# Optimization experiments

Hardware: AMD Instinct MI355X
Metric: run time of the kernel (lower is better)

## Reference

```python
import jax, jax.numpy as jnp
import numpy as np

N, C_IN, C_OUT, H, W = 16, 256, 256, 32, 32
K = 9  # 3x3 kernel


def setup_inputs() -> dict:
    key = jax.random.key(0)
    k1, k2, k3 = jax.random.split(key, 3)
    x = jax.random.normal(k1, (N, C_IN, H, W), dtype=jnp.float32)
    # offsets as produced upstream from anchors: (N, H*W, 18)
    offset = jax.random.normal(k2, (N, H * W, 2 * K), dtype=jnp.float32)
    # DeformConv weight (no bias), kaiming-ish scale
    weight = jax.random.normal(k3, (C_OUT, C_IN, 3, 3), dtype=jnp.float32) * 0.02
    return {"x": x, "offset": offset, "weight": weight}


def _deform_conv3x3(x, offset_nchw, weight):
    """DeformConv v1, kernel 3x3, stride 1, padding 1, dilation 1,
    groups=1, deformable_groups=1, zero padding outside borders."""
    n, c, h, w = x.shape
    o = weight.shape[0]
    # offset channel layout: (dy_k, dx_k) pairs for k = 0..8
    off = offset_nchw.reshape(n, K, 2, h, w)
    dy = off[:, :, 0]  # (N,K,H,W)
    dx = off[:, :, 1]
    ky = (jnp.arange(K) // 3 - 1).astype(x.dtype)  # kernel row offsets -1,0,1
    kx = (jnp.arange(K) % 3 - 1).astype(x.dtype)
    base_y = jnp.arange(h, dtype=x.dtype)[None, None, :, None]
    base_x = jnp.arange(w, dtype=x.dtype)[None, None, None, :]
    py = base_y + ky[None, :, None, None] + dy  # (N,K,H,W) sample rows
    px = base_x + kx[None, :, None, None] + dx  # (N,K,H,W) sample cols

    y0 = jnp.floor(py)
    x0 = jnp.floor(px)
    ly = py - y0  # fractional parts
    lx = px - x0

    x_flat = x.reshape(n, c, h * w)

    def corner(yi, xi, wgt):
        valid = (yi >= 0) & (yi <= h - 1) & (xi >= 0) & (xi <= w - 1)
        yc = jnp.clip(yi, 0, h - 1).astype(jnp.int32)
        xc = jnp.clip(xi, 0, w - 1).astype(jnp.int32)
        idx = (yc * w + xc).reshape(n, K * h * w)
        g = jax.vmap(lambda xf, i: xf[:, i])(x_flat, idx)  # (N,C,K*H*W)
        wv = (wgt * valid.astype(x.dtype)).reshape(n, 1, K * h * w)
        return g * wv

    val = (corner(y0, x0, (1 - ly) * (1 - lx))
           + corner(y0, x0 + 1, (1 - ly) * lx)
           + corner(y0 + 1, x0, ly * (1 - lx))
           + corner(y0 + 1, x0 + 1, ly * lx))
    val = val.reshape(n, c, K, h, w)  # sampled im2col columns
    return jnp.einsum('nckhw,ock->nohw', val, weight.reshape(o, c, K))


def reference(x, offset, weight):
    n, _, h, w = x.shape
    assert h * w == offset.shape[1]
    # AdaptiveConv.forward: (N, HW, 18) -> (N, 18, H, W)
    offset_nchw = jnp.transpose(offset, (0, 2, 1)).reshape(n, 2 * K, h, w)
    return _deform_conv3x3(x, offset_nchw, weight)
```

## Files before the change

kernel.cpp:

```cpp
#include <hip/hip_runtime.h>

#define NB   16
#define CIN  256
#define COUT 256
#define HH   32
#define WW   32
#define HW   1024
#define KK   9
#define CK   2304

typedef __bf16 bf16x8 __attribute__((ext_vector_type(8)));
typedef float  f32x4  __attribute__((ext_vector_type(4)));

__device__ __forceinline__ unsigned short f2bf(float f) {
    unsigned int u = __float_as_uint(f);
    u += 0x7FFFu + ((u >> 16) & 1u);
    return (unsigned short)(u >> 16);
}
__device__ __forceinline__ float bfhi(unsigned int u) {
    return __uint_as_float(u & 0xFFFF0000u);
}
__device__ __forceinline__ float bflo(unsigned int u) {
    return __uint_as_float(u << 16);
}

typedef const __attribute__((address_space(1))) void* gas_ptr;
typedef __attribute__((address_space(3))) void* las_ptr;

__device__ __forceinline__ void async16(const void* g, void* l) {
    __builtin_amdgcn_global_load_lds((gas_ptr)g, (las_ptr)l, 16, 0, 0);
}

__global__ __launch_bounds__(256) void wconv_kernel(const float* __restrict__ w,
                                                    unsigned short* __restrict__ wbf) {
    __shared__ float ls[CK];
    const int o = blockIdx.x;
    const float* wo = w + (size_t)o * CK;
#pragma unroll
    for (int i = threadIdx.x; i < CK; i += 256) ls[i] = wo[i];
    __syncthreads();
    unsigned short* dst = wbf + (size_t)o * CK;
#pragma unroll
    for (int i = threadIdx.x; i < CK; i += 256) {
        int k = i >> 8, c = i & 255;
        dst[i] = f2bf(ls[c * KK + k]);
    }
}

__global__ __launch_bounds__(256) void xt_kernel(const float* __restrict__ x,
                                                 unsigned short* __restrict__ xtb) {
    __shared__ float ls[64][65];
    const int c0  = blockIdx.x * 64;
    const int hw0 = blockIdx.y * 64;
    const int n   = blockIdx.z;
    const int t   = threadIdx.x;
    {
        int c = t >> 2, q = t & 3;
        const float4* base = (const float4*)(x + ((size_t)(n * CIN + c0 + c)) * HW + hw0 + q * 16);
#pragma unroll
        for (int j = 0; j < 4; ++j) {
            float4 v = base[j];
            ls[c][q * 16 + j * 4 + 0] = v.x;
            ls[c][q * 16 + j * 4 + 1] = v.y;
            ls[c][q * 16 + j * 4 + 2] = v.z;
            ls[c][q * 16 + j * 4 + 3] = v.w;
        }
    }
    __syncthreads();
    {
        int hw = t >> 2, seg = (t & 3) * 16;
        unsigned int dw[8];
#pragma unroll
        for (int j = 0; j < 8; ++j) {
            float f0 = ls[seg + 2 * j][hw];
            float f1 = ls[seg + 2 * j + 1][hw];
            dw[j] = (unsigned)f2bf(f0) | ((unsigned)f2bf(f1) << 16);
        }
        uint4* dst = (uint4*)(xtb + ((size_t)(n * HW + hw0 + hw)) * CIN + c0 + seg);
        dst[0] = *(uint4*)&dw[0];
        dst[1] = *(uint4*)&dw[4];
    }
}

__global__ __launch_bounds__(512, 2) void fused_kernel(const unsigned short* __restrict__ wbf,
                                                       const unsigned short* __restrict__ xtb,
                                                       const float* __restrict__ off,
                                                       float* __restrict__ out) {
    __shared__ unsigned short As[2][256 * 64];
    __shared__ unsigned short Bs[2][64 * 64];

    const int tid  = threadIdx.x;
    const int wv   = tid >> 6;
    const int lane = tid & 63;
    const int quad = lane >> 4;
    const int l15  = lane & 15;

    const int hw_local = tid >> 3;
    const int seg      = tid & 7;

    const int id  = blockIdx.x;
    const int n   = ((id & 7) << 1) | ((id >> 3) & 1);
    const int hw0 = (id >> 4) * 64;

    const int hw = hw0 + hw_local;
    const int h  = hw >> 5, w = hw & 31;

    const int srow   = lane >> 3;
    const int schunk = (lane & 7) ^ (srow & 7);

    const uint4*  xb4  = (const uint4*)(xtb + (size_t)n * HW * CIN);
    const float2* offp = (const float2*)(off + ((size_t)n * HW + hw) * (2 * KK));

    f32x4 acc[2][4] = {};

    auto setup = [&](int tap, float wg[4], int ix[4]) {
        float2 o = offp[tap];
        float py = (float)(h + tap / 3 - 1) + o.x;
        float px = (float)(w + tap % 3 - 1) + o.y;
        float y0f = floorf(py), x0f = floorf(px);
        float ly = py - y0f, lx = px - x0f;
        int y0 = (int)y0f, x0 = (int)x0f;
#pragma unroll
        for (int c2 = 0; c2 < 4; ++c2) {
            int yy = y0 + (c2 >> 1);
            int xx = x0 + (c2 & 1);
            float wy = (c2 >> 1) ? ly : 1.0f - ly;
            float wx = (c2 & 1) ? lx : 1.0f - lx;
            bool v = (yy >= 0) && (yy < HH) && (xx >= 0) && (xx < WW);
            wg[c2] = v ? wy * wx : 0.0f;
            int yc = yy < 0 ? 0 : (yy > HH - 1 ? HH - 1 : yy);
            int xc = xx < 0 ? 0 : (xx > WW - 1 ? WW - 1 : xx);
            ix[c2] = yc * WW + xc;
        }
    };

    auto loadc = [&](uint4 cr[4], const int ix[4], int s) {
#pragma unroll
        for (int c2 = 0; c2 < 4; ++c2)
            cr[c2] = xb4[(size_t)ix[c2] * 32 + s * 8 + seg];
    };

    auto build = [&](int nb, int ckb, const uint4 cr[4], const float wg[4]) {
#pragma unroll
        for (int j = 0; j < 4; ++j) {
            int rb = wv * 32 + j * 8;
            async16(wbf + (size_t)(rb + srow) * CK + ckb + schunk * 8, &As[nb][rb * 64]);
        }
        unsigned u0[4], u1[4], u2[4], u3[4];
        *(uint4*)u0 = cr[0]; *(uint4*)u1 = cr[1];
        *(uint4*)u2 = cr[2]; *(uint4*)u3 = cr[3];
        unsigned dw[4];
#pragma unroll
        for (int d = 0; d < 4; ++d) {
            float lo = wg[0] * bflo(u0[d]) + wg[1] * bflo(u1[d])
                     + wg[2] * bflo(u2[d]) + wg[3] * bflo(u3[d]);
            float hi = wg[0] * bfhi(u0[d]) + wg[1] * bfhi(u1[d])
                     + wg[2] * bfhi(u2[d]) + wg[3] * bfhi(u3[d]);
            dw[d] = (unsigned)f2bf(lo) | ((unsigned)f2bf(hi) << 16);
        }
        *(uint4*)&Bs[nb][hw_local * 64 + (seg ^ (hw_local & 7)) * 8] = *(uint4*)dw;
    };

    auto mfma_step = [&](int pb) {
        bf16x8 af[2][2], bfr[4][2];
#pragma unroll
        for (int mi = 0; mi < 2; ++mi)
#pragma unroll
            for (int hh = 0; hh < 2; ++hh) {
                int row = wv * 32 + mi * 16 + l15;
                int ch  = (hh * 4 + quad) ^ (row & 7);
                af[mi][hh] = *(const bf16x8*)&As[pb][row * 64 + ch * 8];
            }
#pragma unroll
        for (int ni = 0; ni < 4; ++ni)
#pragma unroll
            for (int hh = 0; hh < 2; ++hh) {
                int row = ni * 16 + l15;
                int ch  = (hh * 4 + quad) ^ (row & 7);
                bfr[ni][hh] = *(const bf16x8*)&Bs[pb][row * 64 + ch * 8];
            }
#pragma unroll
        for (int mi = 0; mi < 2; ++mi)
#pragma unroll
            for (int ni = 0; ni < 4; ++ni) {
                acc[mi][ni] = __builtin_amdgcn_mfma_f32_16x16x32_bf16(af[mi][0], bfr[ni][0], acc[mi][ni], 0, 0, 0);
                acc[mi][ni] = __builtin_amdgcn_mfma_f32_16x16x32_bf16(af[mi][1], bfr[ni][1], acc[mi][ni], 0, 0, 0);
            }
    };

    float wgc[4], wgn[4];
    int   ixc[4], ixn[4];
    uint4 crA[4], crB[4];

    setup(0, wgc, ixc);
    loadc(crA, ixc, 0);
    build(0, 0, crA, wgc);
    loadc(crB, ixc, 1);
    __syncthreads();

    for (int tap = 0; tap < 9; ++tap) {
        const int ckb = tap * 256;
        build(1, ckb + 64, crB, wgc);
        loadc(crA, ixc, 2);
        mfma_step(0);
        __syncthreads();
        build(0, ckb + 128, crA, wgc);
        loadc(crB, ixc, 3);
        mfma_step(1);
        __syncthreads();
        build(1, ckb + 192, crB, wgc);
        if (tap < 8) { setup(tap + 1, wgn, ixn); loadc(crA, ixn, 0); }
        mfma_step(0);
        __syncthreads();
        if (tap < 8) {
            build(0, ckb + 256, crA, wgn);
            loadc(crB, ixn, 1);
#pragma unroll
            for (int c2 = 0; c2 < 4; ++c2) { wgc[c2] = wgn[c2]; ixc[c2] = ixn[c2]; }
            mfma_step(1);
            __syncthreads();
        } else {
            mfma_step(1);
        }
    }

    float* opnt = out + (size_t)n * COUT * HW + hw0;
#pragma unroll
    for (int mi = 0; mi < 2; ++mi)
#pragma unroll
        for (int ni = 0; ni < 4; ++ni) {
            int col = ni * 16 + l15;
#pragma unroll
            for (int rr = 0; rr < 4; ++rr) {
                int row = wv * 32 + mi * 16 + quad * 4 + rr;
                opnt[(size_t)row * HW + col] = acc[mi][ni][rr];
            }
        }
}

extern "C" void kernel_launch(void* const* d_in, const int* in_sizes, int n_in,
                              void* d_out, int out_size, void* d_ws, size_t ws_size,
                              hipStream_t stream) {
    const float* x   = (const float*)d_in[0];
    const float* off = (const float*)d_in[1];
    const float* wt  = (const float*)d_in[2];
    float* out = (float*)d_out;

    unsigned short* wbf = (unsigned short*)d_ws;
    unsigned short* xtb = (unsigned short*)((char*)d_ws + 1179648);

    wconv_kernel<<<256, 256, 0, stream>>>(wt, wbf);
    xt_kernel<<<dim3(4, 16, 16), 256, 0, stream>>>(x, xtb);
    fused_kernel<<<256, 512, 0, stream>>>(wbf, xtb, off, out);
}
```

Measured before the change: 122.3 us.

## Split fused deform-conv kernel into producer and consumer wavefronts

The 8 wavefronts of each block are split into roles. Four producer waves do the offset setup, bilinear gather, B-tile build and async A-tile loads, and four consumer waves run only MFMAs, each covering 64 output rows instead of 32. The goal is to overlap gather and build latency with matrix math through warp specialization. In exchange, each consumer wave doubles its accumulator and fragment registers, only half the waves issue MFMAs, and producers hold eight uint4 prefetch registers per stage.

```diff
diff --git a/kernel.cpp b/kernel.cpp
--- a/kernel.cpp
+++ b/kernel.cpp
@@ -92,28 +92,34 @@
     const int tid  = threadIdx.x;
     const int wv   = tid >> 6;
     const int lane = tid & 63;
-    const int quad = lane >> 4;
-    const int l15  = lane & 15;
-
-    const int hw_local = tid >> 3;
-    const int seg      = tid & 7;
 
     const int id  = blockIdx.x;
     const int n   = ((id & 7) << 1) | ((id >> 3) & 1);
     const int hw0 = (id >> 4) * 64;
 
-    const int hw = hw0 + hw_local;
-    const int h  = hw >> 5, w = hw & 31;
-
+    const bool producer = (wv >= 4);
+
+    const int quad = lane >> 4;
+    const int l15  = lane & 15;
+    f32x4 acc[4][4] = {};
+
+    const int ptid = (wv - 4) * 64 + lane;
+    const int hwl  = ptid >> 2;
+    const int segq = ptid & 3;
+    const int hw   = hw0 + (hwl & 63);
+    const int h    = hw >> 5, w = hw & 31;
+    const int pv   = wv - 4;
     const int srow   = lane >> 3;
     const int schunk = (lane & 7) ^ (srow & 7);
 
     const uint4*  xb4  = (const uint4*)(xtb + (size_t)n * HW * CIN);
     const float2* offp = (const float2*)(off + ((size_t)n * HW + hw) * (2 * KK));
 
-    f32x4 acc[2][4] = {};
-
-    auto setup = [&](int tap, float wg[4], int ix[4]) {
+    float wgs0[4], wgs1[4];
+    uint4 crs0[8], crs1[8];
+
+    auto prefetch = [&](int t, float* wg, uint4* cr) {
+        int tap = t >> 2, sub = t & 3;
         float2 o = offp[tap];
         float py = (float)(h + tap / 3 - 1) + o.x;
         float px = (float)(w + tap % 3 - 1) + o.y;
@@ -130,44 +136,45 @@
             wg[c2] = v ? wy * wx : 0.0f;
             int yc = yy < 0 ? 0 : (yy > HH - 1 ? HH - 1 : yy);
             int xc = xx < 0 ? 0 : (xx > WW - 1 ? WW - 1 : xx);
-            ix[c2] = yc * WW + xc;
+            int ridx = yc * WW + xc;
+            const uint4* rp = xb4 + (size_t)ridx * 32 + sub * 8 + segq * 2;
+            cr[2 * c2]     = rp[0];
+            cr[2 * c2 + 1] = rp[1];
         }
     };
 
-    auto loadc = [&](uint4 cr[4], const int ix[4], int s) {
-#pragma unroll
-        for (int c2 = 0; c2 < 4; ++c2)
-            cr[c2] = xb4[(size_t)ix[c2] * 32 + s * 8 + seg];
+    auto build = [&](int nb, int t, const float* wg, const uint4* cr) {
+#pragma unroll
+        for (int p = 0; p < 2; ++p) {
+            unsigned u0[4], u1[4], u2[4], u3[4];
+            *(uint4*)u0 = cr[0 + p]; *(uint4*)u1 = cr[2 + p];
+            *(uint4*)u2 = cr[4 + p]; *(uint4*)u3 = cr[6 + p];
+            unsigned dw[4];
+#pragma unroll
+            for (int d = 0; d < 4; ++d) {
+                float lo = wg[0] * bflo(u0[d]) + wg[1] * bflo(u1[d])
+                         + wg[2] * bflo(u2[d]) + wg[3] * bflo(u3[d]);
+                float hi = wg[0] * bfhi(u0[d]) + wg[1] * bfhi(u1[d])
+                         + wg[2] * bfhi(u2[d]) + wg[3] * bfhi(u3[d]);
+                dw[d] = (unsigned)f2bf(lo) | ((unsigned)f2bf(hi) << 16);
+            }
+            *(uint4*)&Bs[nb][hwl * 64 + ((segq * 2 + p) ^ (hwl & 7)) * 8] = *(uint4*)dw;
+        }
+#pragma unroll
+        for (int j = 0; j < 8; ++j) {
+            int rb = pv * 64 + j * 8;
+            async16(wbf + (size_t)(rb + srow) * CK + t * 64 + schunk * 8,
+                    &As[nb][rb * 64]);
+        }
     };
 
-    auto build = [&](int nb, int ckb, const uint4 cr[4], const float wg[4]) {
-#pragma unroll
-        for (int j = 0; j < 4; ++j) {
-            int rb = wv * 32 + j * 8;
-            async16(wbf + (size_t)(rb + srow) * CK + ckb + schunk * 8, &As[nb][rb * 64]);
-        }
-        unsigned u0[4], u1[4], u2[4], u3[4];
-        *(uint4*)u0 = cr[0]; *(uint4*)u1 = cr[1];
-        *(uint4*)u2 = cr[2]; *(uint4*)u3 = cr[3];
-        unsigned dw[4];
-#pragma unroll
-        for (int d = 0; d < 4; ++d) {
-            float lo = wg[0] * bflo(u0[d]) + wg[1] * bflo(u1[d])
-                     + wg[2] * bflo(u2[d]) + wg[3] * bflo(u3[d]);
-            float hi = wg[0] * bfhi(u0[d]) + wg[1] * bfhi(u1[d])
-                     + wg[2] * bfhi(u2[d]) + wg[3] * bfhi(u3[d]);
-            dw[d] = (unsigned)f2bf(lo) | ((unsigned)f2bf(hi) << 16);
-        }
-        *(uint4*)&Bs[nb][hw_local * 64 + (seg ^ (hw_local & 7)) * 8] = *(uint4*)dw;
-    };
-
     auto mfma_step = [&](int pb) {
-        bf16x8 af[2][2], bfr[4][2];
-#pragma unroll
-        for (int mi = 0; mi < 2; ++mi)
+        bf16x8 af[4][2], bfr[4][2];
+#pragma unroll
+        for (int mi = 0; mi < 4; ++mi)
 #pragma unroll
             for (int hh = 0; hh < 2; ++hh) {
-                int row = wv * 32 + mi * 16 + l15;
+                int row = wv * 64 + mi * 16 + l15;
                 int ch  = (hh * 4 + quad) ^ (row & 7);
                 af[mi][hh] = *(const bf16x8*)&As[pb][row * 64 + ch * 8];
             }
@@ -180,7 +187,7 @@
                 bfr[ni][hh] = *(const bf16x8*)&Bs[pb][row * 64 + ch * 8];
             }
 #pragma unroll
-        for (int mi = 0; mi < 2; ++mi)
+        for (int mi = 0; mi < 4; ++mi)
 #pragma unroll
             for (int ni = 0; ni < 4; ++ni) {
                 acc[mi][ni] = __builtin_amdgcn_mfma_f32_16x16x32_bf16(af[mi][0], bfr[ni][0], acc[mi][ni], 0, 0, 0);
@@ -188,54 +195,45 @@
             }
     };
 
-    float wgc[4], wgn[4];
-    int   ixc[4], ixn[4];
-    uint4 crA[4], crB[4];
-
-    setup(0, wgc, ixc);
-    loadc(crA, ixc, 0);
-    build(0, 0, crA, wgc);
-    loadc(crB, ixc, 1);
+    if (producer) {
+        prefetch(0, wgs0, crs0);
+        build(0, 0, wgs0, crs0);
+        prefetch(1, wgs1, crs1);
+    }
     __syncthreads();
 
-    for (int tap = 0; tap < 9; ++tap) {
-        const int ckb = tap * 256;
-        build(1, ckb + 64, crB, wgc);
-        loadc(crA, ixc, 2);
-        mfma_step(0);
+    for (int sp = 0; sp < 18; ++sp) {
+        const int s = sp * 2;
+        if (producer) {
+            if (s < 35) build(1, s + 1, wgs1, crs1);
+            if (s + 2 < 36) prefetch(s + 2, wgs0, crs0);
+        } else {
+            mfma_step(0);
+        }
         __syncthreads();
-        build(0, ckb + 128, crA, wgc);
-        loadc(crB, ixc, 3);
-        mfma_step(1);
-        __syncthreads();
-        build(1, ckb + 192, crB, wgc);
-        if (tap < 8) { setup(tap + 1, wgn, ixn); loadc(crA, ixn, 0); }
-        mfma_step(0);
-        __syncthreads();
-        if (tap < 8) {
-            build(0, ckb + 256, crA, wgn);
-            loadc(crB, ixn, 1);
-#pragma unroll
-            for (int c2 = 0; c2 < 4; ++c2) { wgc[c2] = wgn[c2]; ixc[c2] = ixn[c2]; }
-            mfma_step(1);
-            __syncthreads();
+        if (producer) {
+            if (s + 2 < 36) build(0, s + 2, wgs0, crs0);
+            if (s + 3 < 36) prefetch(s + 3, wgs1, crs1);
         } else {
             mfma_step(1);
         }
-    }
-
-    float* opnt = out + (size_t)n * COUT * HW + hw0;
-#pragma unroll
-    for (int mi = 0; mi < 2; ++mi)
-#pragma unroll
-        for (int ni = 0; ni < 4; ++ni) {
-            int col = ni * 16 + l15;
-#pragma unroll
-            for (int rr = 0; rr < 4; ++rr) {
-                int row = wv * 32 + mi * 16 + quad * 4 + rr;
-                opnt[(size_t)row * HW + col] = acc[mi][ni][rr];
-            }
-        }
+        __syncthreads();
+    }
+
+    if (!producer) {
+        float* opnt = out + (size_t)n * COUT * HW + hw0;
+#pragma unroll
+        for (int mi = 0; mi < 4; ++mi)
+#pragma unroll
+            for (int ni = 0; ni < 4; ++ni) {
+                int col = ni * 16 + l15;
+#pragma unroll
+                for (int rr = 0; rr < 4; ++rr) {
+                    int row = wv * 64 + mi * 16 + quad * 4 + rr;
+                    opnt[(size_t)row * HW + col] = acc[mi][ni][rr];
+                }
+            }
+    }
 }
 
 extern "C" void kernel_launch(void* const* d_in, const int* in_sizes, int n_in,
```

New measurement: 136.3 us. 11.5% more time.

## Load weight fragments directly from global into registers instead of LDS staging

Applied to the files above, without the earlier changes.

Removes the LDS A-tile buffers and the async global-to-LDS copies of bf16 weights. Each wave now loads its MFMA A fragments straight from global memory into registers, double-buffered across the pipeline steps. This cuts LDS traffic and shared memory use, which may allow more occupancy. In exchange each wave issues uncoalesced-ish 16-byte global loads per step and relies on L2/L1 hits for weight reuse across blocks. The bf16 packing also switches to the HIP intrinsic __float22bfloat162_rn.

```diff
diff --git a/kernel.cpp b/kernel.cpp
--- a/kernel.cpp
+++ b/kernel.cpp
@@ -1,4 +1,5 @@
 #include <hip/hip_runtime.h>
+#include <hip/hip_bf16.h>
 
 #define NB   16
 #define CIN  256
@@ -22,13 +23,6 @@
 }
 __device__ __forceinline__ float bflo(unsigned int u) {
     return __uint_as_float(u << 16);
-}
-
-typedef const __attribute__((address_space(1))) void* gas_ptr;
-typedef __attribute__((address_space(3))) void* las_ptr;
-
-__device__ __forceinline__ void async16(const void* g, void* l) {
-    __builtin_amdgcn_global_load_lds((gas_ptr)g, (las_ptr)l, 16, 0, 0);
 }
 
 __global__ __launch_bounds__(256) void wconv_kernel(const float* __restrict__ w,
@@ -86,7 +80,6 @@
                                                        const unsigned short* __restrict__ xtb,
                                                        const float* __restrict__ off,
                                                        float* __restrict__ out) {
-    __shared__ unsigned short As[2][256 * 64];
     __shared__ unsigned short Bs[2][64 * 64];
 
     const int tid  = threadIdx.x;
@@ -95,21 +88,19 @@
     const int quad = lane >> 4;
     const int l15  = lane & 15;
 
-    const int hw_local = tid >> 3;
-    const int seg      = tid & 7;
+    const int hwl = tid >> 3;
+    const int seg = tid & 7;
 
     const int id  = blockIdx.x;
     const int n   = ((id & 7) << 1) | ((id >> 3) & 1);
     const int hw0 = (id >> 4) * 64;
 
-    const int hw = hw0 + hw_local;
+    const int hw = hw0 + hwl;
     const int h  = hw >> 5, w = hw & 31;
-
-    const int srow   = lane >> 3;
-    const int schunk = (lane & 7) ^ (srow & 7);
 
     const uint4*  xb4  = (const uint4*)(xtb + (size_t)n * HW * CIN);
     const float2* offp = (const float2*)(off + ((size_t)n * HW + hw) * (2 * KK));
+    const unsigned short* Abase = wbf + (size_t)(wv * 32 + l15) * CK + quad * 8;
 
     f32x4 acc[2][4] = {};
 
@@ -135,42 +126,41 @@
     };
 
     auto loadc = [&](uint4 cr[4], const int ix[4], int s) {
+        int sub = s & 3;
 #pragma unroll
         for (int c2 = 0; c2 < 4; ++c2)
-            cr[c2] = xb4[(size_t)ix[c2] * 32 + s * 8 + seg];
-    };
-
-    auto build = [&](int nb, int ckb, const uint4 cr[4], const float wg[4]) {
-#pragma unroll
-        for (int j = 0; j < 4; ++j) {
-            int rb = wv * 32 + j * 8;
-            async16(wbf + (size_t)(rb + srow) * CK + ckb + schunk * 8, &As[nb][rb * 64]);
-        }
+            cr[c2] = xb4[(size_t)ix[c2] * 32 + sub * 8 + seg];
+    };
+
+    auto loada = [&](bf16x8 af[2][2], int s) {
+        const unsigned short* p = Abase + s * 64;
+#pragma unroll
+        for (int mi = 0; mi < 2; ++mi)
+#pragma unroll
+            for (int hh = 0; hh < 2; ++hh)
+                af[mi][hh] = *(const bf16x8*)(p + (size_t)mi * 16 * CK + hh * 32);
+    };
+
+    auto buildB = [&](int nb, const uint4 cr[4], const float wg[4]) {
         unsigned u0[4], u1[4], u2[4], u3[4];
         *(uint4*)u0 = cr[0]; *(uint4*)u1 = cr[1];
         *(uint4*)u2 = cr[2]; *(uint4*)u3 = cr[3];
         unsigned dw[4];
 #pragma unroll
         for (int d = 0; d < 4; ++d) {
-            float lo = wg[0] * bflo(u0[d]) + wg[1] * bflo(u1[d])
-                     + wg[2] * bflo(u2[d]) + wg[3] * bflo(u3[d]);
-            float hi = wg[0] * bfhi(u0[d]) + wg[1] * bfhi(u1[d])
-                     + wg[2] * bfhi(u2[d]) + wg[3] * bfhi(u3[d]);
-            dw[d] = (unsigned)f2bf(lo) | ((unsigned)f2bf(hi) << 16);
-        }
-        *(uint4*)&Bs[nb][hw_local * 64 + (seg ^ (hw_local & 7)) * 8] = *(uint4*)dw;
-    };
-
-    auto mfma_step = [&](int pb) {
-        bf16x8 af[2][2], bfr[4][2];
-#pragma unroll
-        for (int mi = 0; mi < 2; ++mi)
-#pragma unroll
-            for (int hh = 0; hh < 2; ++hh) {
-                int row = wv * 32 + mi * 16 + l15;
-                int ch  = (hh * 4 + quad) ^ (row & 7);
-                af[mi][hh] = *(const bf16x8*)&As[pb][row * 64 + ch * 8];
-            }
+            float2 lv;
+            lv.x = wg[0] * bflo(u0[d]) + wg[1] * bflo(u1[d])
+                 + wg[2] * bflo(u2[d]) + wg[3] * bflo(u3[d]);
+            lv.y = wg[0] * bfhi(u0[d]) + wg[1] * bfhi(u1[d])
+                 + wg[2] * bfhi(u2[d]) + wg[3] * bfhi(u3[d]);
+            __hip_bfloat162 bb = __float22bfloat162_rn(lv);
+            dw[d] = *(unsigned*)&bb;
+        }
+        *(uint4*)&Bs[nb][hwl * 64 + (seg ^ (hwl & 7)) * 8] = *(uint4*)dw;
+    };
+
+    auto mfma_step = [&](int pb, const bf16x8 af[2][2]) {
+        bf16x8 bfr[4][2];
 #pragma unroll
         for (int ni = 0; ni < 4; ++ni)
 #pragma unroll
@@ -190,37 +180,43 @@
 
     float wgc[4], wgn[4];
     int   ixc[4], ixn[4];
-    uint4 crA[4], crB[4];
+    uint4 crE[4], crO[4];
+    bf16x8 afE[2][2], afO[2][2];
 
     setup(0, wgc, ixc);
-    loadc(crA, ixc, 0);
-    build(0, 0, crA, wgc);
-    loadc(crB, ixc, 1);
+    loadc(crE, ixc, 0);
+    loadc(crO, ixc, 1);
+    loada(afE, 0);
+    buildB(0, crE, wgc);
     __syncthreads();
 
     for (int tap = 0; tap < 9; ++tap) {
-        const int ckb = tap * 256;
-        build(1, ckb + 64, crB, wgc);
-        loadc(crA, ixc, 2);
-        mfma_step(0);
+        const int b = tap * 4;
+        buildB(1, crO, wgc);
+        loadc(crE, ixc, b + 2);
+        loada(afO, b + 1);
+        mfma_step(0, afE);
         __syncthreads();
-        build(0, ckb + 128, crA, wgc);
-        loadc(crB, ixc, 3);
-        mfma_step(1);
+        buildB(0, crE, wgc);
+        loadc(crO, ixc, b + 3);
+        loada(afE, b + 2);
+        mfma_step(1, afO);
         __syncthreads();
-        build(1, ckb + 192, crB, wgc);
-        if (tap < 8) { setup(tap + 1, wgn, ixn); loadc(crA, ixn, 0); }
-        mfma_step(0);
+        buildB(1, crO, wgc);
+        if (tap < 8) { setup(tap + 1, wgn, ixn); loadc(crE, ixn, b + 4); }
+        loada(afO, b + 3);
+        mfma_step(0, afE);
         __syncthreads();
         if (tap < 8) {
-            build(0, ckb + 256, crA, wgn);
-            loadc(crB, ixn, 1);
+            buildB(0, crE, wgn);
+            loadc(crO, ixn, b + 5);
+            loada(afE, b + 4);
 #pragma unroll
             for (int c2 = 0; c2 < 4; ++c2) { wgc[c2] = wgn[c2]; ixc[c2] = ixn[c2]; }
-            mfma_step(1);
+            mfma_step(1, afO);
             __syncthreads();
         } else {
-            mfma_step(1);
+            mfma_step(1, afO);
         }
     }
 
```

New measurement: 127.1 us. 1.04x slower.
